# Kernel optimization log

Measured on AMD Instinct MI355X. Metric: run time of the kernel, lower is better.

## Reference

```python
import jax, jax.numpy as jnp
import numpy as np

ALPHA = 0.25
GAMMA = 2.0
W_CLASS = 2.0
W_BBOX = 5.0
W_GIOU = 2.0
EPS = 1e-8

BS, Q, NUM_CLASSES, M_PER_IMG = 16, 900, 80, 100


def box_cxcywh_to_xyxy(b):
    cx, cy, w, h = jnp.split(b, 4, axis=-1)
    return jnp.concatenate([cx - 0.5 * w, cy - 0.5 * h, cx + 0.5 * w, cy + 0.5 * h], axis=-1)


def box_xyxy_to_cxcywh(b):
    x1, y1, x2, y2 = jnp.split(b, 4, axis=-1)
    return jnp.concatenate([(x1 + x2) * 0.5, (y1 + y2) * 0.5, x2 - x1, y2 - y1], axis=-1)


def generalized_box_iou(a, b):
    # a: [N,4], b: [M,4], xyxy -> [N,M] GIoU
    area_a = (a[:, 2] - a[:, 0]) * (a[:, 3] - a[:, 1])
    area_b = (b[:, 2] - b[:, 0]) * (b[:, 3] - b[:, 1])
    lt = jnp.maximum(a[:, None, :2], b[None, :, :2])
    rb = jnp.minimum(a[:, None, 2:], b[None, :, 2:])
    wh = jnp.clip(rb - lt, 0.0)
    inter = wh[..., 0] * wh[..., 1]
    union = area_a[:, None] + area_b[None, :] - inter
    iou = inter / union
    lt_c = jnp.minimum(a[:, None, :2], b[None, :, :2])
    rb_c = jnp.maximum(a[:, None, 2:], b[None, :, 2:])
    wh_c = jnp.clip(rb_c - lt_c, 0.0)
    area_c = wh_c[..., 0] * wh_c[..., 1]
    return iou - (area_c - union) / area_c


def setup_inputs() -> dict:
    key = jax.random.key(0)
    k1, k2, k3, k4 = jax.random.split(key, 4)
    pred_logits = jax.random.normal(k1, (BS, Q, NUM_CLASSES), dtype=jnp.float32)
    pred_boxes = jax.random.uniform(k2, (BS, Q, 4), dtype=jnp.float32)  # cxcywh in (0,1)
    T = BS * M_PER_IMG
    tgt_cxcywh = jax.random.uniform(k3, (T, 4), dtype=jnp.float32)
    # keep widths/heights in a sane positive range, produce valid xyxy
    tgt_cxcywh = tgt_cxcywh.at[:, 2:].set(0.05 + 0.5 * tgt_cxcywh[:, 2:])
    tgt_boxes = box_cxcywh_to_xyxy(tgt_cxcywh)
    tgt_labels = jax.random.randint(k4, (T,), 0, NUM_CLASSES, dtype=jnp.int64)
    return {"pred_logits": pred_logits, "pred_boxes": pred_boxes,
            "tgt_boxes": tgt_boxes, "tgt_labels": tgt_labels}


def reference(pred_logits, pred_boxes, tgt_boxes, tgt_labels):
    bs, q, _ = pred_logits.shape
    out_prob = jax.nn.sigmoid(pred_logits.reshape(bs * q, -1))  # [NQ, C]
    out_bbox = pred_boxes.reshape(bs * q, 4)                    # [NQ, 4] cxcywh
    # focal-style classification cost
    neg_cost = (1.0 - ALPHA) * out_prob ** GAMMA * (-jnp.log(1.0 - out_prob + EPS))
    pos_cost = ALPHA * (1.0 - out_prob) ** GAMMA * (-jnp.log(out_prob + EPS))
    cost_class = (pos_cost - neg_cost)[:, tgt_labels]           # [NQ, T]
    # L1 cost in cxcywh space
    tgt_cxcywh = box_xyxy_to_cxcywh(tgt_boxes)
    cost_bbox = jnp.sum(jnp.abs(out_bbox[:, None, :] - tgt_cxcywh[None, :, :]), axis=-1)
    # GIoU cost in xyxy space
    cost_giou = -generalized_box_iou(box_cxcywh_to_xyxy(out_bbox), tgt_boxes)
    C = W_BBOX * cost_bbox + W_CLASS * cost_class + W_GIOU * cost_giou
    return C.reshape(bs, q, -1)  # [bs, Q, T_total]; per-image block i is C[i, :, i*M:(i+1)*M]
```

## Files before the change

### kernel.cpp

```cpp
#include <hip/hip_runtime.h>
#include <math.h>


#define NCLS  80
#define QTILE 4
#define NTHR  256

typedef float v2f __attribute__((ext_vector_type(2)));

static __device__ __forceinline__ v2f v2(float a, float b) { v2f r; r.x = a; r.y = b; return r; }

__global__ __launch_bounds__(NTHR)
void matcher_cost_kernel(const float* __restrict__ logits,
                         const float* __restrict__ pboxes,
                         const float* __restrict__ tboxes,
                         const int*   __restrict__ tlabels,
                         float* __restrict__ out,
                         int NQ, int T)
{
    __shared__ float ccT[NCLS][QTILE];

    const int tid = threadIdx.x;
    const int q0  = blockIdx.x * QTILE;

    for (int i = tid; i < QTILE * NCLS; i += NTHR) {
        int q = i / NCLS, lab = i - q * NCLS;
        float x = logits[(size_t)q0 * NCLS + i];
        float p = 1.0f / (1.0f + __expf(-x));
        float pos = 0.25f * (1.0f - p) * (1.0f - p) * (-__logf(p + 1e-8f));
        float neg = 0.75f * p * p * (-__logf(1.0f - p + 1e-8f));
        ccT[lab][q] = 2.0f * (pos - neg) + 2.0f;
    }

    float qcx[QTILE], qcy[QTILE], qw[QTILE], qh[QTILE];
    float qwh[QTILE], qhh[QTILE], qa[QTILE];
#pragma unroll
    for (int q = 0; q < QTILE; ++q) {
        float4 pb = reinterpret_cast<const float4*>(pboxes)[q0 + q];
        qcx[q] = pb.x; qcy[q] = pb.y; qw[q] = pb.z; qh[q] = pb.w;
        qwh[q] = 0.5f * pb.z; qhh[q] = 0.5f * pb.w;
        qa[q]  = pb.z * pb.w;
    }
    __syncthreads();

    const float4* tb4 = reinterpret_cast<const float4*>(tboxes);
    const int2*   lb2 = reinterpret_cast<const int2*>(tlabels);
    const float4* ccv = reinterpret_cast<const float4*>(ccT);

    const int npair = T >> 1;
    float2* obase = reinterpret_cast<float2*>(out) + (size_t)q0 * npair;

    int pair = tid;
    float4 b0 = tb4[pair * 2], b1 = tb4[pair * 2 + 1];
    int2 L = lb2[pair];

    for (;;) {
        const int  nxt  = pair + NTHR;
        const bool more = nxt < npair;
        const int  nc   = more ? nxt : pair;
        float4 nb0 = tb4[nc * 2], nb1 = tb4[nc * 2 + 1];
        int2   nL  = lb2[nc];

        float4 c0 = ccv[L.x], c1 = ccv[L.y];

        v2f bX1 = v2(b0.x, b1.x), bY1 = v2(b0.y, b1.y);
        v2f bX2 = v2(b0.z, b1.z), bY2 = v2(b0.w, b1.w);
        v2f bw  = bX2 - bX1,      bh  = bY2 - bY1;
        v2f bcx = 0.5f * (bX1 + bX2);
        v2f bcy = 0.5f * (bY1 + bY2);
        v2f ba  = bw * bh;
        v2f bwh = 0.5f * bw,      bhh = 0.5f * bh;

#pragma unroll
        for (int q = 0; q < QTILE; ++q) {
            v2f dcx = qcx[q] - bcx, dcy = qcy[q] - bcy;
            v2f dw  = qw[q]  - bw,  dh  = qh[q]  - bh;
            v2f adx = v2(fabsf(dcx.x), fabsf(dcx.y));
            v2f ady = v2(fabsf(dcy.x), fabsf(dcy.y));
            v2f l1  = (adx + ady) + v2(fabsf(dw.x) + fabsf(dh.x),
                                       fabsf(dw.y) + fabsf(dh.y));

            v2f hw  = qwh[q] + bwh,  hh  = qhh[q] + bhh;
            v2f dwh = qwh[q] - bwh,  dhh = qhh[q] - bhh;
            v2f ewx = v2(fmaxf(adx.x, fabsf(dwh.x)), fmaxf(adx.y, fabsf(dwh.y)));
            v2f ewy = v2(fmaxf(ady.x, fabsf(dhh.x)), fmaxf(ady.y, fabsf(dhh.y)));
            v2f iwd = hw - ewx,      ihd = hh - ewy;
            v2f iw  = v2(fmaxf(iwd.x, 0.f), fmaxf(iwd.y, 0.f));
            v2f ih  = v2(fmaxf(ihd.x, 0.f), fmaxf(ihd.y, 0.f));
            v2f inter = iw * ih;
            v2f uni = (qa[q] + ba) - inter;
            v2f cw = 2.0f * hw - iwd;
            v2f ch = 2.0f * hh - ihd;
            v2f ca = cw * ch;

            float clsa = (q == 0) ? c0.x : (q == 1) ? c0.y : (q == 2) ? c0.z : c0.w;
            float clsb = (q == 0) ? c1.x : (q == 1) ? c1.y : (q == 2) ? c1.z : c1.w;

            v2f base = 5.0f * l1 + v2(clsa, clsb);
            v2f den  = uni * ca;
            v2f r    = v2(__builtin_amdgcn_rcpf(den.x),
                          __builtin_amdgcn_rcpf(den.y));
            v2f num  = uni * uni + inter * ca;
            v2f res  = -2.0f * (num * r) + base;

            obase[q * npair + pair] = make_float2(res.x, res.y);
        }

        if (!more) break;
        pair = nxt; b0 = nb0; b1 = nb1; L = nL;
    }
}

extern "C" void kernel_launch(void* const* d_in, const int* in_sizes, int n_in,
                              void* d_out, int out_size, void* d_ws, size_t ws_size,
                              hipStream_t stream) {
    const float* logits  = (const float*)d_in[0];
    const float* pboxes  = (const float*)d_in[1];
    const float* tboxes  = (const float*)d_in[2];
    const int*   tlabels = (const int*)d_in[3];
    float* out = (float*)d_out;

    const int NQ = in_sizes[1] / 4;
    const int T  = in_sizes[2] / 4;

    const int nblocks = (NQ + QTILE - 1) / QTILE;
    matcher_cost_kernel<<<nblocks, NTHR, 0, stream>>>(logits, pboxes, tboxes,
                                                      tlabels, out, NQ, T);
}
```

Measured before the change: 31.18 us.

## Process four targets per thread with 16-byte nontemporal stores, halve block size

Each thread now handles four target boxes per iteration instead of two and writes them as one 16-byte vector with a nontemporal store hint. The block size drops from 256 to 128 threads, which matches T/4 = 400 quads more closely, so fewer threads sit idle in the last loop pass. The aim is fewer, wider store instructions and less cache pollution from the large output write. In exchange, register pressure per thread goes up and the kernel now assumes T is divisible by four.

```diff
diff --git a/kernel.cpp b/kernel.cpp
--- a/kernel.cpp
+++ b/kernel.cpp
@@ -4,11 +4,47 @@
 
 #define NCLS  80
 #define QTILE 4
-#define NTHR  256
+#define NTHR  128
 
 typedef float v2f __attribute__((ext_vector_type(2)));
+typedef float v4f __attribute__((ext_vector_type(4)));
 
 static __device__ __forceinline__ v2f v2(float a, float b) { v2f r; r.x = a; r.y = b; return r; }
+
+static __device__ __forceinline__ v2f cost_pair(
+    float qcx, float qcy, float qw, float qh, float qwh, float qhh, float qa,
+    v2f bcx, v2f bcy, v2f bw, v2f bh, v2f bwh, v2f bhh, v2f ba, v2f cls)
+{
+    v2f dcx = qcx - bcx, dcy = qcy - bcy;
+    v2f dw  = qw  - bw,  dh  = qh  - bh;
+    float l1x = (fabsf(dcx.x) + fabsf(dcy.x)) + (fabsf(dw.x) + fabsf(dh.x));
+    float l1y = (fabsf(dcx.y) + fabsf(dcy.y)) + (fabsf(dw.y) + fabsf(dh.y));
+
+    v2f hw  = qwh + bwh,  hh  = qhh + bhh;
+    v2f dwh = qwh - bwh,  dhh = qhh - bhh;
+    v2f ew = v2(fmaxf(fabsf(dcx.x), fabsf(dwh.x)),
+                fmaxf(fabsf(dcx.y), fabsf(dwh.y)));
+    v2f eh = v2(fmaxf(fabsf(dcy.x), fabsf(dhh.x)),
+                fmaxf(fabsf(dcy.y), fabsf(dhh.y)));
+    v2f iwd = hw - ew, ihd = hh - eh;
+    v2f iw = v2(fmaxf(iwd.x, 0.f), fmaxf(iwd.y, 0.f));
+    v2f ih = v2(fmaxf(ihd.x, 0.f), fmaxf(ihd.y, 0.f));
+    v2f inter = iw * ih;
+    v2f uni = (qa + ba) - inter;
+    v2f cw = 2.0f * hw - iwd, ch = 2.0f * hh - ihd;
+    v2f ca = cw * ch;
+
+    v2f base = 5.0f * v2(l1x, l1y) + cls;
+    v2f den  = uni * ca;
+    v2f r    = v2(__builtin_amdgcn_rcpf(den.x),
+                  __builtin_amdgcn_rcpf(den.y));
+    v2f num  = uni * uni + inter * ca;
+    return -2.0f * (num * r) + base;
+}
+
+static __device__ __forceinline__ float qsel(float4 c, int q) {
+    return (q == 0) ? c.x : (q == 1) ? c.y : (q == 2) ? c.z : c.w;
+}
 
 __global__ __launch_bounds__(NTHR)
 void matcher_cost_kernel(const float* __restrict__ logits,
@@ -44,70 +80,53 @@
     __syncthreads();
 
     const float4* tb4 = reinterpret_cast<const float4*>(tboxes);
-    const int2*   lb2 = reinterpret_cast<const int2*>(tlabels);
+    const int4*   lb4 = reinterpret_cast<const int4*>(tlabels);
     const float4* ccv = reinterpret_cast<const float4*>(ccT);
 
-    const int npair = T >> 1;
-    float2* obase = reinterpret_cast<float2*>(out) + (size_t)q0 * npair;
+    const int nquad = T >> 2;
+    v4f* obase = reinterpret_cast<v4f*>(out) + (size_t)q0 * nquad;
 
-    int pair = tid;
-    float4 b0 = tb4[pair * 2], b1 = tb4[pair * 2 + 1];
-    int2 L = lb2[pair];
+    int quad = tid;
+    float4 b0 = tb4[4 * quad],     b1 = tb4[4 * quad + 1];
+    float4 b2 = tb4[4 * quad + 2], b3 = tb4[4 * quad + 3];
+    int4 L = lb4[quad];
 
     for (;;) {
-        const int  nxt  = pair + NTHR;
-        const bool more = nxt < npair;
-        const int  nc   = more ? nxt : pair;
-        float4 nb0 = tb4[nc * 2], nb1 = tb4[nc * 2 + 1];
-        int2   nL  = lb2[nc];
+        const int  nxt  = quad + NTHR;
+        const bool more = nxt < nquad;
+        const int  nc   = more ? nxt : quad;
+        float4 nb0 = tb4[4 * nc],     nb1 = tb4[4 * nc + 1];
+        float4 nb2 = tb4[4 * nc + 2], nb3 = tb4[4 * nc + 3];
+        int4   nL  = lb4[nc];
 
-        float4 c0 = ccv[L.x], c1 = ccv[L.y];
+        float4 c0 = ccv[L.x], c1 = ccv[L.y], c2 = ccv[L.z], c3 = ccv[L.w];
 
-        v2f bX1 = v2(b0.x, b1.x), bY1 = v2(b0.y, b1.y);
-        v2f bX2 = v2(b0.z, b1.z), bY2 = v2(b0.w, b1.w);
-        v2f bw  = bX2 - bX1,      bh  = bY2 - bY1;
-        v2f bcx = 0.5f * (bX1 + bX2);
-        v2f bcy = 0.5f * (bY1 + bY2);
-        v2f ba  = bw * bh;
-        v2f bwh = 0.5f * bw,      bhh = 0.5f * bh;
+        v2f aX1 = v2(b0.x, b1.x), aY1 = v2(b0.y, b1.y);
+        v2f aX2 = v2(b0.z, b1.z), aY2 = v2(b0.w, b1.w);
+        v2f bX1 = v2(b2.x, b3.x), bY1 = v2(b2.y, b3.y);
+        v2f bX2 = v2(b2.z, b3.z), bY2 = v2(b2.w, b3.w);
+
+        v2f aw  = aX2 - aX1, ah = aY2 - aY1;
+        v2f acx = 0.5f * (aX1 + aX2), acy = 0.5f * (aY1 + aY2);
+        v2f aa  = aw * ah, awh = 0.5f * aw, ahh = 0.5f * ah;
+        v2f bw  = bX2 - bX1, bh = bY2 - bY1;
+        v2f bcx = 0.5f * (bX1 + bX2), bcy = 0.5f * (bY1 + bY2);
+        v2f ba  = bw * bh, bwh = 0.5f * bw, bhh = 0.5f * bh;
 
 #pragma unroll
         for (int q = 0; q < QTILE; ++q) {
-            v2f dcx = qcx[q] - bcx, dcy = qcy[q] - bcy;
-            v2f dw  = qw[q]  - bw,  dh  = qh[q]  - bh;
-            v2f adx = v2(fabsf(dcx.x), fabsf(dcx.y));
-            v2f ady = v2(fabsf(dcy.x), fabsf(dcy.y));
-            v2f l1  = (adx + ady) + v2(fabsf(dw.x) + fabsf(dh.x),
-                                       fabsf(dw.y) + fabsf(dh.y));
-
-            v2f hw  = qwh[q] + bwh,  hh  = qhh[q] + bhh;
-            v2f dwh = qwh[q] - bwh,  dhh = qhh[q] - bhh;
-            v2f ewx = v2(fmaxf(adx.x, fabsf(dwh.x)), fmaxf(adx.y, fabsf(dwh.y)));
-            v2f ewy = v2(fmaxf(ady.x, fabsf(dhh.x)), fmaxf(ady.y, fabsf(dhh.y)));
-            v2f iwd = hw - ewx,      ihd = hh - ewy;
-            v2f iw  = v2(fmaxf(iwd.x, 0.f), fmaxf(iwd.y, 0.f));
-            v2f ih  = v2(fmaxf(ihd.x, 0.f), fmaxf(ihd.y, 0.f));
-            v2f inter = iw * ih;
-            v2f uni = (qa[q] + ba) - inter;
-            v2f cw = 2.0f * hw - iwd;
-            v2f ch = 2.0f * hh - ihd;
-            v2f ca = cw * ch;
-
-            float clsa = (q == 0) ? c0.x : (q == 1) ? c0.y : (q == 2) ? c0.z : c0.w;
-            float clsb = (q == 0) ? c1.x : (q == 1) ? c1.y : (q == 2) ? c1.z : c1.w;
-
-            v2f base = 5.0f * l1 + v2(clsa, clsb);
-            v2f den  = uni * ca;
-            v2f r    = v2(__builtin_amdgcn_rcpf(den.x),
-                          __builtin_amdgcn_rcpf(den.y));
-            v2f num  = uni * uni + inter * ca;
-            v2f res  = -2.0f * (num * r) + base;
-
-            obase[q * npair + pair] = make_float2(res.x, res.y);
+            v2f rA = cost_pair(qcx[q], qcy[q], qw[q], qh[q], qwh[q], qhh[q], qa[q],
+                               acx, acy, aw, ah, awh, ahh, aa,
+                               v2(qsel(c0, q), qsel(c1, q)));
+            v2f rB = cost_pair(qcx[q], qcy[q], qw[q], qh[q], qwh[q], qhh[q], qa[q],
+                               bcx, bcy, bw, bh, bwh, bhh, ba,
+                               v2(qsel(c2, q), qsel(c3, q)));
+            v4f res; res.x = rA.x; res.y = rA.y; res.z = rB.x; res.w = rB.y;
+            __builtin_nontemporal_store(res, obase + q * nquad + quad);
         }
 
         if (!more) break;
-        pair = nxt; b0 = nb0; b1 = nb1; L = nL;
+        quad = nxt; b0 = nb0; b1 = nb1; b2 = nb2; b3 = nb3; L = nL;
     }
 }
 
```

After: 32.82 us. +5.2%, slower.
